# Kernel optimization log

Measured on AMD Instinct MI355X. Metric: run time of the kernel, lower is better.

Reference implementation:

```python
import jax, jax.numpy as jnp
import numpy as np

# Model dims (match init_kwargs cfg)
B, C_IN, L = 16, 3, 1024
D_MODEL, N_LAYERS = 256, 4
D_STATE, D_CONV, EXPAND = 16, 4, 2
D_INNER = EXPAND * D_MODEL            # 512
DT_RANK = (D_MODEL + 15) // 16        # 16 (mamba_ssm 'auto' rank)


def setup_inputs() -> dict:
    key = jax.random.key(0)
    ks = jax.random.split(key, 10)
    def rn(k, shape, scale):
        return jax.random.normal(k, shape, jnp.float32) * scale
    inp = {
        "x": jax.random.normal(ks[0], (B, C_IN, L), jnp.float32),
        # input stem: Conv1d(3 -> d_model, k=3, pad=1)
        "stem_w": rn(ks[1], (D_MODEL, C_IN, 3), 0.3),
        "stem_b": jnp.zeros((D_MODEL,), jnp.float32),
        # per-layer params, stacked on leading layer dim
        "norm_g": jnp.ones((N_LAYERS, D_MODEL), jnp.float32),
        "norm_b": jnp.zeros((N_LAYERS, D_MODEL), jnp.float32),
        "in_proj_w": rn(ks[2], (N_LAYERS, 2 * D_INNER, D_MODEL), 0.02),
        "conv_w": rn(ks[3], (N_LAYERS, D_INNER, D_CONV), 0.2),
        "conv_b": jnp.zeros((N_LAYERS, D_INNER), jnp.float32),
        "x_proj_w": rn(ks[4], (N_LAYERS, DT_RANK + 2 * D_STATE, D_INNER), 0.02),
        "dt_w": rn(ks[5], (N_LAYERS, D_INNER, DT_RANK), 0.05),
        "dt_b": jnp.full((N_LAYERS, D_INNER), -4.6, jnp.float32),  # softplus ~= 0.01
        "A_log": jnp.log(jnp.broadcast_to(
            jnp.arange(1, D_STATE + 1, dtype=jnp.float32), (N_LAYERS, D_INNER, D_STATE))),
        "Dp": jnp.ones((N_LAYERS, D_INNER), jnp.float32),
        "out_w": rn(ks[6], (N_LAYERS, D_MODEL, D_INNER), 0.02),
        # final norm + output head Conv1d(d_model -> 1, k=1)
        "fnorm_g": jnp.ones((D_MODEL,), jnp.float32),
        "fnorm_b": jnp.zeros((D_MODEL,), jnp.float32),
        "head_w": rn(ks[7], (1, D_MODEL), 0.05),
        "head_b": jnp.zeros((1,), jnp.float32),
    }
    return inp


def _layernorm(x, g, b, eps=1e-5):
    mu = jnp.mean(x, axis=-1, keepdims=True)
    var = jnp.mean((x - mu) ** 2, axis=-1, keepdims=True)
    return (x - mu) * jax.lax.rsqrt(var + eps) * g + b


def _silu(x):
    return x * jax.nn.sigmoid(x)


def _selective_scan(u, delta, A, Bm, Cm, D):
    # u, delta: [B, L, di]; Bm, Cm: [B, L, ds]; A: [di, ds]; D: [di]
    # h_t = exp(delta_t * A) * h_{t-1} + (delta_t * u_t) * B_t ; y_t = <C_t, h_t>
    def step(h, t):
        d_t, B_t, C_t, u_t = t  # [B,di], [B,ds], [B,ds], [B,di]
        h = h * jnp.exp(d_t[..., None] * A) + (d_t * u_t)[..., None] * B_t[:, None, :]
        return h, jnp.einsum('bds,bs->bd', h, C_t)
    h0 = jnp.zeros((u.shape[0], A.shape[0], A.shape[1]), u.dtype)
    xs = (jnp.moveaxis(delta, 1, 0), jnp.moveaxis(Bm, 1, 0),
          jnp.moveaxis(Cm, 1, 0), jnp.moveaxis(u, 1, 0))
    _, ys = jax.lax.scan(step, h0, xs)            # ys: [L, B, di]
    return jnp.moveaxis(ys, 0, 1) + u * D


def _mamba(x, in_w, cw, cb, xw, dtw, dtb, A_log, Dp, ow):
    # x: [B, L, d_model]
    xz = jnp.einsum('bld,ed->ble', x, in_w)       # [B, L, 2*di]
    xin, z = jnp.split(xz, 2, axis=-1)
    # causal depthwise conv over time
    xc = jnp.moveaxis(xin, 1, 2)                  # [B, di, L]
    xc = jax.lax.conv_general_dilated(
        xc, cw[:, None, :], (1,), [(D_CONV - 1, 0)],
        feature_group_count=D_INNER,
        dimension_numbers=('NCH', 'OIH', 'NCH')) + cb[None, :, None]
    xin = _silu(jnp.moveaxis(xc, 1, 2))           # [B, L, di]
    proj = jnp.einsum('bld,ed->ble', xin, xw)     # [B, L, dt_rank + 2*ds]
    dt = proj[..., :DT_RANK]
    Bm = proj[..., DT_RANK:DT_RANK + D_STATE]
    Cm = proj[..., DT_RANK + D_STATE:]
    delta = jax.nn.softplus(jnp.einsum('blr,dr->bld', dt, dtw) + dtb)
    A = -jnp.exp(A_log)
    y = _selective_scan(xin, delta, A, Bm, Cm, Dp)
    y = y * _silu(z)
    return jnp.einsum('bld,od->blo', y, ow)       # [B, L, d_model]


def reference(x, stem_w, stem_b, norm_g, norm_b, in_proj_w, conv_w, conv_b,
              x_proj_w, dt_w, dt_b, A_log, Dp, out_w, fnorm_g, fnorm_b,
              head_w, head_b):
    # stem: Conv1d(k=3, same padding) + ReLU
    h = jax.lax.conv_general_dilated(
        x, stem_w, (1,), [(1, 1)],
        dimension_numbers=('NCH', 'OIH', 'NCH')) + stem_b[None, :, None]
    h = jax.nn.relu(h)
    h = jnp.moveaxis(h, 1, 2)                     # [B, L, d_model]
    for i in range(N_LAYERS):
        h = h + _mamba(_layernorm(h, norm_g[i], norm_b[i]),
                       in_proj_w[i], conv_w[i], conv_b[i], x_proj_w[i],
                       dt_w[i], dt_b[i], A_log[i], Dp[i], out_w[i])
    h = _layernorm(h, fnorm_g, fnorm_b)
    out = jnp.einsum('bld,od->blo', h, head_w) + head_b
    return jax.nn.sigmoid(jnp.moveaxis(out, 1, 2))  # [B, 1, L]
```

## Files before the change

kernel.cpp:

```cpp
#include <hip/hip_runtime.h>
#include <math.h>

#define BSZ 16
#define LQ 1024
#define DM 256
#define DI 512
#define NT (BSZ*LQ)

typedef __attribute__((ext_vector_type(8))) short short8;
typedef __attribute__((ext_vector_type(4))) short short4v;
typedef __attribute__((ext_vector_type(4))) float f32x4;

#define AS1(p) (const __attribute__((address_space(1))) void*)(p)
#define AS3(p) (__attribute__((address_space(3))) void*)(p)
#define GLOAD16(g, l) __builtin_amdgcn_global_load_lds(AS1(g), AS3(l), 16, 0, 0)

__device__ __forceinline__ short f2bf(float f) {
  union { float f; unsigned u; } a; a.f = f;
  unsigned r = (a.u + 0x7FFF + ((a.u >> 16) & 1)) >> 16;
  return (short)r;
}
__device__ __forceinline__ float bf2f(short s) {
  union { unsigned u; float f; } a; a.u = ((unsigned)(unsigned short)s) << 16;
  return a.f;
}

__global__ void stem_kernel(const float* __restrict__ x, const float* __restrict__ w,
                            const float* __restrict__ bias, float* __restrict__ h) {
  int idx = blockIdx.x * 256 + threadIdx.x;
  int d = idx & 255;
  int l = (idx >> 8) & 1023;
  int b = idx >> 18;
  float acc = bias[d];
#pragma unroll
  for (int c = 0; c < 3; c++) {
    const float* xr = x + (size_t)(b * 3 + c) * LQ;
    const float* wr = w + (size_t)(d * 3 + c) * 3;
#pragma unroll
    for (int k = 0; k < 3; k++) {
      int t = l + k - 1;
      if (t >= 0 && t < LQ) acc += xr[t] * wr[k];
    }
  }
  h[idx] = fmaxf(acc, 0.f);
}

#define WB_IN 262144
#define WB_XP 65536
#define WB_OUT 131072
#define WB_L (WB_IN + WB_XP + WB_OUT)

__global__ void convert_w(const float* __restrict__ in_w, const float* __restrict__ xp_w,
                          const float* __restrict__ out_w, short* __restrict__ wb) {
  int layer = blockIdx.y;
  int idx = blockIdx.x * 256 + threadIdx.x;
  short* dst = wb + (size_t)layer * WB_L;
  float v;
  if (idx < WB_IN) {
    v = in_w[(size_t)layer * WB_IN + idx];
  } else if (idx < WB_IN + WB_XP) {
    int k = idx - WB_IN; int row = k >> 9, col = k & 511;
    v = (row < 48) ? xp_w[(size_t)layer * 48 * 512 + row * 512 + col] : 0.f;
  } else {
    int k = idx - WB_IN - WB_XP;
    v = out_w[(size_t)layer * WB_OUT + k];
  }
  dst[idx] = f2bf(v);
}

__global__ void ln_kernel(const float* __restrict__ x, const float* __restrict__ g,
                          const float* __restrict__ bv, short* __restrict__ o) {
  int token = blockIdx.x * 4 + (threadIdx.x >> 6);
  int lane = threadIdx.x & 63;
  f32x4 v = *(const f32x4*)(x + (size_t)token * DM + lane * 4);
  float s = v[0] + v[1] + v[2] + v[3];
  float q = v[0]*v[0] + v[1]*v[1] + v[2]*v[2] + v[3]*v[3];
#pragma unroll
  for (int off = 32; off > 0; off >>= 1) {
    s += __shfl_xor(s, off, 64);
    q += __shfl_xor(q, off, 64);
  }
  float mu = s * (1.f / DM);
  float var = q * (1.f / DM) - mu * mu;
  float rs = rsqrtf(var + 1e-5f);
  f32x4 gg = *(const f32x4*)(g + lane * 4);
  f32x4 bb = *(const f32x4*)(bv + lane * 4);
  short4v ov;
#pragma unroll
  for (int k = 0; k < 4; k++) ov[k] = f2bf((v[k] - mu) * rs * gg[k] + bb[k]);
  *(short4v*)(o + (size_t)token * DM + lane * 4) = ov;
}

__global__ __launch_bounds__(256) void gemm_mfma_s16(
    const short* __restrict__ A, int K,
    const short* __restrict__ W,
    short* __restrict__ C0, int ld0,
    short* __restrict__ C1, int ld1,
    int split, int N) {
  __shared__ short As[128 * 32];
  __shared__ short Bs[128 * 32];
  int tid = threadIdx.x;
  int wave = tid >> 6, lane = tid & 63;
  int bm = blockIdx.y * 128, bn = blockIdx.x * 128;
  int wm = (wave >> 1) * 64, wn = (wave & 1) * 64;

  f32x4 acc[4][4];
#pragma unroll
  for (int i = 0; i < 4; i++)
#pragma unroll
    for (int j = 0; j < 4; j++) { acc[i][j][0] = 0.f; acc[i][j][1] = 0.f; acc[i][j][2] = 0.f; acc[i][j][3] = 0.f; }

  int srow = lane >> 2;
  int scol = (lane & 3) * 8;
  const short* Ag = A + (size_t)(bm + wave * 32 + srow) * K + scol;
  const short* Wg = W + (size_t)(bn + wave * 32 + srow) * K + scol;
  short* AsW = As + wave * 32 * 32;
  short* BsW = Bs + wave * 32 * 32;

  int fr = lane & 15;
  int kg = (lane >> 4) * 8;

  for (int k0 = 0; k0 < K; k0 += 32) {
    GLOAD16(Ag + k0,                    AsW);
    GLOAD16(Ag + k0 + (size_t)16 * K,   AsW + 16 * 32);
    GLOAD16(Wg + k0,                    BsW);
    GLOAD16(Wg + k0 + (size_t)16 * K,   BsW + 16 * 32);
    __syncthreads();

    short8 af[4], bf[4];
#pragma unroll
    for (int i = 0; i < 4; i++) af[i] = *(const short8*)&As[(wm + i * 16 + fr) * 32 + kg];
#pragma unroll
    for (int j = 0; j < 4; j++) bf[j] = *(const short8*)&Bs[(wn + j * 16 + fr) * 32 + kg];
#pragma unroll
    for (int i = 0; i < 4; i++)
#pragma unroll
      for (int j = 0; j < 4; j++)
        acc[i][j] = __builtin_amdgcn_mfma_f32_16x16x32_bf16(af[i], bf[j], acc[i][j], 0, 0, 0);
    __syncthreads();
  }

  int cn = lane & 15, cr = (lane >> 4) * 4;
#pragma unroll
  for (int i = 0; i < 4; i++) {
    int row0 = bm + wm + i * 16 + cr;
#pragma unroll
    for (int j = 0; j < 4; j++) {
      int col = bn + wn + j * 16 + cn;
      if (col < N) {
#pragma unroll
        for (int r = 0; r < 4; r++) {
          short* p = (col < split) ? (C0 + (size_t)(row0 + r) * ld0 + col)
                                   : (C1 + (size_t)(row0 + r) * ld1 + (col - split));
          *p = f2bf(acc[i][j][r]);
        }
      }
    }
  }
}

__global__ __launch_bounds__(256) void gemm_mfma64(
    const short* __restrict__ A, int K,
    const short* __restrict__ W,
    float* __restrict__ C, int ldc, int N, int accum) {
  __shared__ short As[64 * 64];
  __shared__ short Bs[64 * 64];
  int tid = threadIdx.x;
  int wave = tid >> 6, lane = tid & 63;
  int bm = blockIdx.y * 64, bn = blockIdx.x * 64;
  int wm = (wave >> 1) * 32, wn = (wave & 1) * 32;

  f32x4 acc[2][2];
#pragma unroll
  for (int i = 0; i < 2; i++)
#pragma unroll
    for (int j = 0; j < 2; j++) { acc[i][j][0] = 0.f; acc[i][j][1] = 0.f; acc[i][j][2] = 0.f; acc[i][j][3] = 0.f; }

  const short* Ag = A + (size_t)bm * K;
  const short* Wg = W + (size_t)bn * K;
  int fr = lane & 15;
  int kg = (lane >> 4) * 8;

  for (int k0 = 0; k0 < K; k0 += 64) {
#pragma unroll
    for (int i = 0; i < 2; i++) {
      int c = tid + i * 256;
      int row = c >> 3, kk = (c & 7) * 8;
      GLOAD16(Ag + (size_t)row * K + k0 + kk, As + c * 8);
      GLOAD16(Wg + (size_t)row * K + k0 + kk, Bs + c * 8);
    }
    __syncthreads();

#pragma unroll
    for (int ks = 0; ks < 2; ks++) {
      short8 af[2], bf[2];
#pragma unroll
      for (int i = 0; i < 2; i++) af[i] = *(const short8*)&As[(wm + i * 16 + fr) * 64 + ks * 32 + kg];
#pragma unroll
      for (int j = 0; j < 2; j++) bf[j] = *(const short8*)&Bs[(wn + j * 16 + fr) * 64 + ks * 32 + kg];
#pragma unroll
      for (int i = 0; i < 2; i++)
#pragma unroll
        for (int j = 0; j < 2; j++)
          acc[i][j] = __builtin_amdgcn_mfma_f32_16x16x32_bf16(af[i], bf[j], acc[i][j], 0, 0, 0);
    }
    __syncthreads();
  }

  int cn = lane & 15, cr = (lane >> 4) * 4;
#pragma unroll
  for (int i = 0; i < 2; i++) {
    int row0 = bm + wm + i * 16 + cr;
#pragma unroll
    for (int j = 0; j < 2; j++) {
      int col = bn + wn + j * 16 + cn;
      if (col < N) {
#pragma unroll
        for (int r = 0; r < 4; r++) {
          float v = acc[i][j][r];
          float* p = C + (size_t)(row0 + r) * ldc + col;
          if (accum) v += *p;
          *p = v;
        }
      }
    }
  }
}

__global__ void conv_silu_kernel(const short* __restrict__ xcb, const float* __restrict__ cw,
                                 const float* __restrict__ cb, short* __restrict__ xinb) {
  int idx = blockIdx.x * 256 + threadIdx.x;
  int d = idx & 511;
  int l = (idx >> 9) & 1023;
  int b = idx >> 19;
  float acc = cb[d];
  const short* base = xcb + (size_t)b * LQ * 512 + d;
#pragma unroll
  for (int k = 0; k < 4; k++) {
    int t = l + k - 3;
    if (t >= 0) acc += bf2f(base[(size_t)t * 512]) * cw[d * 4 + k];
  }
  float s = acc / (1.f + __expf(-acc));
  xinb[idx] = f2bf(s);
}

template <int CTRL>
__device__ __forceinline__ float dpp_add(float x) {
  int yi = __builtin_amdgcn_update_dpp(0, __float_as_int(x), CTRL, 0xF, 0xF, true);
  return x + __int_as_float(yi);
}
__device__ __forceinline__ float sum16(float x) {
  x = dpp_add<0xB1>(x);
  x = dpp_add<0x4E>(x);
  x = dpp_add<0x124>(x);
  x = dpp_add<0x128>(x);
  return x;
}

#define TCH 32
__global__ __launch_bounds__(256) void scan_kernel(
    const short* __restrict__ xinb, const float* __restrict__ proj,
    const short* __restrict__ zc,
    const float* __restrict__ dt_w, const float* __restrict__ dt_b,
    const float* __restrict__ A_log, const float* __restrict__ Dp,
    short* __restrict__ ybf) {
  int b  = blockIdx.x >> 5;
  int d0 = (blockIdx.x & 31) << 4;
  int tid = threadIdx.x;
  int ci = tid >> 4;
  int s  = tid & 15;
  int d = d0 + ci;

  __shared__ float sDt[32 * 20];
  __shared__ float sBT[16 * 36];
  __shared__ float sCT[16 * 36];
  __shared__ float sUT[16 * 36];
  __shared__ float sDU[16 * 36];
  __shared__ float sDel[16 * 36];
  __shared__ float sY[32 * 17];

  float Av = -__expf(A_log[(size_t)d * 16 + s]);
  f32x4 wv4[4];
#pragma unroll
  for (int k = 0; k < 4; k++) wv4[k] = *(const f32x4*)&dt_w[(size_t)d * 16 + k * 4];
  float db = dt_b[d];
  float Ddj = Dp[d0 + s];
  float h = 0.f;

  const float* projb = proj + (size_t)b * LQ * 48;
  const short* xinbb = xinb + (size_t)b * LQ * 512 + d0;
  const short* zcb   = zc   + (size_t)b * LQ * 512 + d0;
  short* ybb         = ybf  + (size_t)b * LQ * 512 + d0;

  int tt = tid >> 4, j = tid & 15;

  int tr[6], rr[6];
#pragma unroll
  for (int k = 0; k < 6; k++) { int idx = tid + k * 256; tr[k] = idx / 48; rr[k] = idx - tr[k] * 48; }

  float uv0, uv1, zv0, zv1;
  {
    float pjv[6];
#pragma unroll
    for (int k = 0; k < 6; k++) pjv[k] = projb[tid + k * 256];
    uv0 = bf2f(xinbb[(size_t)tt * 512 + j]);
    uv1 = bf2f(xinbb[(size_t)(tt + 16) * 512 + j]);
    zv0 = bf2f(zcb[(size_t)tt * 512 + j]);
    zv1 = bf2f(zcb[(size_t)(tt + 16) * 512 + j]);
#pragma unroll
    for (int k = 0; k < 6; k++) {
      int r = rr[k], t = tr[k];
      if (r < 16)      sDt[t * 20 + r] = pjv[k];
      else if (r < 32) sBT[(r - 16) * 36 + t] = pjv[k];
      else             sCT[(r - 32) * 36 + t] = pjv[k];
    }
    sUT[j * 36 + tt] = uv0;
    sUT[j * 36 + tt + 16] = uv1;
  }
  __syncthreads();

  const int NCH = LQ / TCH;
  for (int c = 0; c < NCH; c++) {
    int t0 = c * TCH;

    float pjn[6], un0 = 0.f, un1 = 0.f, zn0 = 0.f, zn1 = 0.f;
    if (c + 1 < NCH) {
      const float* g = projb + (t0 + TCH) * 48;
#pragma unroll
      for (int k = 0; k < 6; k++) pjn[k] = g[tid + k * 256];
      un0 = bf2f(xinbb[(size_t)(t0 + TCH + tt) * 512 + j]);
      un1 = bf2f(xinbb[(size_t)(t0 + TCH + tt + 16) * 512 + j]);
      zn0 = bf2f(zcb[(size_t)(t0 + TCH + tt) * 512 + j]);
      zn1 = bf2f(zcb[(size_t)(t0 + TCH + tt + 16) * 512 + j]);
    }

    {
      f32x4 a0 = *(const f32x4*)&sDt[s * 20 + 0];
      f32x4 a1 = *(const f32x4*)&sDt[s * 20 + 4];
      f32x4 a2 = *(const f32x4*)&sDt[s * 20 + 8];
      f32x4 a3 = *(const f32x4*)&sDt[s * 20 + 12];
      f32x4 b0 = *(const f32x4*)&sDt[(s + 16) * 20 + 0];
      f32x4 b1 = *(const f32x4*)&sDt[(s + 16) * 20 + 4];
      f32x4 b2 = *(const f32x4*)&sDt[(s + 16) * 20 + 8];
      f32x4 b3 = *(const f32x4*)&sDt[(s + 16) * 20 + 12];
      float dt0 = db, dt1 = db;
#pragma unroll
      for (int q = 0; q < 4; q++) {
        dt0 += a0[q] * wv4[0][q] + a1[q] * wv4[1][q] + a2[q] * wv4[2][q] + a3[q] * wv4[3][q];
        dt1 += b0[q] * wv4[0][q] + b1[q] * wv4[1][q] + b2[q] * wv4[2][q] + b3[q] * wv4[3][q];
      }
      float de0 = (dt0 > 15.f) ? dt0 : __logf(1.f + __expf(dt0));
      float de1 = (dt1 > 15.f) ? dt1 : __logf(1.f + __expf(dt1));
      float u0 = sUT[ci * 36 + s];
      float u1 = sUT[ci * 36 + s + 16];
      sDel[ci * 36 + s]      = de0;
      sDel[ci * 36 + s + 16] = de1;
      sDU[ci * 36 + s]       = de0 * u0;
      sDU[ci * 36 + s + 16]  = de1 * u1;
    }
    __syncthreads();

    {
      float ee[TCH], cin[TCH];
      f32x4 ct[8];
      {
        f32x4 dl[8], du8[8], bt[8];
#pragma unroll
        for (int k = 0; k < 8; k++) {
          dl[k]  = *(const f32x4*)&sDel[ci * 36 + k * 4];
          du8[k] = *(const f32x4*)&sDU[ci * 36 + k * 4];
          bt[k]  = *(const f32x4*)&sBT[s * 36 + k * 4];
          ct[k]  = *(const f32x4*)&sCT[s * 36 + k * 4];
        }
#pragma unroll
        for (int t = 0; t < TCH; t++) {
          ee[t] = __expf(dl[t >> 2][t & 3] * Av);
          cin[t] = du8[t >> 2][t & 3] * bt[t >> 2][t & 3];
        }
      }
      float pv0 = 0.f, pv1 = 0.f;
#pragma unroll
      for (int t = 0; t < TCH; t++) {
        h = h * ee[t] + cin[t];
        float p = sum16(h * ct[t >> 2][t & 3]);
        if (t < 16) pv0 = (s == t) ? p : pv0;
        else        pv1 = (s == (t - 16)) ? p : pv1;
      }
      sY[s * 17 + ci] = pv0;
      sY[(s + 16) * 17 + ci] = pv1;
    }
    __syncthreads();

    {
      float p0 = sY[tt * 17 + j];
      float p1 = sY[(tt + 16) * 17 + j];
      float y0 = p0 + uv0 * Ddj;
      float y1 = p1 + uv1 * Ddj;
      float g0 = zv0 / (1.f + __expf(-zv0));
      float g1 = zv1 / (1.f + __expf(-zv1));
      ybb[(size_t)(t0 + tt) * 512 + j] = f2bf(y0 * g0);
      ybb[(size_t)(t0 + tt + 16) * 512 + j] = f2bf(y1 * g1);
    }
    if (c + 1 < NCH) {
#pragma unroll
      for (int k = 0; k < 6; k++) {
        int r = rr[k], t = tr[k];
        if (r < 16)      sDt[t * 20 + r] = pjn[k];
        else if (r < 32) sBT[(r - 16) * 36 + t] = pjn[k];
        else             sCT[(r - 32) * 36 + t] = pjn[k];
      }
      sUT[j * 36 + tt] = un0;
      sUT[j * 36 + tt + 16] = un1;
      uv0 = un0; uv1 = un1; zv0 = zn0; zv1 = zn1;
    }
    __syncthreads();
  }
}

__global__ void head_kernel(const float* __restrict__ h, const float* __restrict__ g,
                            const float* __restrict__ bv, const float* __restrict__ hw,
                            const float* __restrict__ hb, float* __restrict__ out) {
  int token = blockIdx.x;
  int d = threadIdx.x;
  float v = h[(size_t)token * DM + d];
  float s = v, q = v * v;
#pragma unroll
  for (int off = 32; off > 0; off >>= 1) {
    s += __shfl_down(s, off, 64);
    q += __shfl_down(q, off, 64);
  }
  __shared__ float ss[4], qq[4], cc[4];
  int lane = d & 63, wid = d >> 6;
  if (lane == 0) { ss[wid] = s; qq[wid] = q; }
  __syncthreads();
  s = ss[0] + ss[1] + ss[2] + ss[3];
  q = qq[0] + qq[1] + qq[2] + qq[3];
  float mu = s * (1.f / DM);
  float var = q * (1.f / DM) - mu * mu;
  float rs = rsqrtf(var + 1e-5f);
  float xn = (v - mu) * rs * g[d] + bv[d];
  float c = xn * hw[d];
#pragma unroll
  for (int off = 32; off > 0; off >>= 1) c += __shfl_down(c, off, 64);
  if (lane == 0) cc[wid] = c;
  __syncthreads();
  if (threadIdx.x == 0) {
    float t = cc[0] + cc[1] + cc[2] + cc[3] + hb[0];
    out[token] = 1.f / (1.f + __expf(-t));
  }
}

extern "C" void kernel_launch(void* const* d_in, const int* in_sizes, int n_in,
                              void* d_out, int out_size, void* d_ws, size_t ws_size,
                              hipStream_t stream) {
  const float* x        = (const float*)d_in[0];
  const float* stem_w   = (const float*)d_in[1];
  const float* stem_b   = (const float*)d_in[2];
  const float* norm_g   = (const float*)d_in[3];
  const float* norm_b   = (const float*)d_in[4];
  const float* in_proj_w= (const float*)d_in[5];
  const float* conv_w   = (const float*)d_in[6];
  const float* conv_b   = (const float*)d_in[7];
  const float* x_proj_w = (const float*)d_in[8];
  const float* dt_w     = (const float*)d_in[9];
  const float* dt_b     = (const float*)d_in[10];
  const float* A_log    = (const float*)d_in[11];
  const float* Dp       = (const float*)d_in[12];
  const float* out_w    = (const float*)d_in[13];
  const float* fnorm_g  = (const float*)d_in[14];
  const float* fnorm_b  = (const float*)d_in[15];
  const float* head_w   = (const float*)d_in[16];
  const float* head_b   = (const float*)d_in[17];

  char* base = (char*)d_ws;
  float* h    = (float*)(base);
  short* xcb  = (short*)(base + ((size_t)16 << 20));
  short* zcb  = (short*)(base + ((size_t)32 << 20));
  short* xnb  = (short*)(base + ((size_t)48 << 20));
  short* xinb = (short*)(base + ((size_t)56 << 20));
  short* ybf  = (short*)(base + ((size_t)72 << 20));
  float* proj = (float*)(base + ((size_t)88 << 20));
  short* wb   = (short*)(base + ((size_t)91 << 20));

  stem_kernel<<<NT, 256, 0, stream>>>(x, stem_w, stem_b, h);

  dim3 gcw(WB_L / 256, 4);
  convert_w<<<gcw, 256, 0, stream>>>(in_proj_w, x_proj_w, out_w, wb);

  for (int i = 0; i < 4; i++) {
    const short* wbl = wb + (size_t)i * WB_L;

    ln_kernel<<<NT / 4, 256, 0, stream>>>(h, norm_g + i * DM, norm_b + i * DM, xnb);

    dim3 g1(8, NT / 128);
    gemm_mfma_s16<<<g1, 256, 0, stream>>>(xnb, 256, wbl, xcb, 512, zcb, 512, 512, 1024);

    conv_silu_kernel<<<NT * DI / 256, 256, 0, stream>>>(xcb, conv_w + i * DI * 4,
                                                        conv_b + i * DI, xinb);

    dim3 g2(1, NT / 64);
    gemm_mfma64<<<g2, 256, 0, stream>>>(xinb, 512, wbl + WB_IN, proj, 48, 48, 0);

    scan_kernel<<<512, 256, 0, stream>>>(xinb, proj, zcb,
                                         dt_w + (size_t)i * DI * 16, dt_b + i * DI,
                                         A_log + (size_t)i * DI * 16, Dp + i * DI, ybf);

    dim3 g3(4, NT / 64);
    gemm_mfma64<<<g3, 256, 0, stream>>>(ybf, 512, wbl + WB_IN + WB_XP, h, 256, 256, 1);
  }

  head_kernel<<<NT, 256, 0, stream>>>(h, fnorm_g, fnorm_b, head_w, head_b, (float*)d_out);
}
```

Before: 875.3 us.

## Fuse LayerNorm into in_proj GEMM and causal conv+SiLU into x_proj GEMM

Drops the standalone LayerNorm and depthwise conv kernels. The in_proj GEMM now normalizes its 128-row tile of h straight into a full-K LDS buffer. The x_proj GEMM now computes the 4-tap causal conv plus SiLU per tile, feeding the MFMAs from LDS and also writing xinb for the scan. This removes the xnb round trip and the separate conv pass over xcb. The cost is that each of the 8 column blocks of GEMM1 recomputes LN and re-reads its rows of h, and the larger LDS footprint (about 75KB) may lower occupancy. The x_proj weight buffer is shrunk to 64 padded rows to match.

```diff
diff --git a/kernel.cpp b/kernel.cpp
--- a/kernel.cpp
+++ b/kernel.cpp
@@ -46,7 +46,7 @@
 }
 
 #define WB_IN 262144
-#define WB_XP 65536
+#define WB_XP 32768
 #define WB_OUT 131072
 #define WB_L (WB_IN + WB_XP + WB_OUT)
 
@@ -68,68 +68,73 @@
   dst[idx] = f2bf(v);
 }
 
-__global__ void ln_kernel(const float* __restrict__ x, const float* __restrict__ g,
-                          const float* __restrict__ bv, short* __restrict__ o) {
-  int token = blockIdx.x * 4 + (threadIdx.x >> 6);
-  int lane = threadIdx.x & 63;
-  f32x4 v = *(const f32x4*)(x + (size_t)token * DM + lane * 4);
-  float s = v[0] + v[1] + v[2] + v[3];
-  float q = v[0]*v[0] + v[1]*v[1] + v[2]*v[2] + v[3]*v[3];
-#pragma unroll
-  for (int off = 32; off > 0; off >>= 1) {
-    s += __shfl_xor(s, off, 64);
-    q += __shfl_xor(q, off, 64);
-  }
-  float mu = s * (1.f / DM);
-  float var = q * (1.f / DM) - mu * mu;
-  float rs = rsqrtf(var + 1e-5f);
-  f32x4 gg = *(const f32x4*)(g + lane * 4);
-  f32x4 bb = *(const f32x4*)(bv + lane * 4);
-  short4v ov;
-#pragma unroll
-  for (int k = 0; k < 4; k++) ov[k] = f2bf((v[k] - mu) * rs * gg[k] + bb[k]);
-  *(short4v*)(o + (size_t)token * DM + lane * 4) = ov;
-}
-
-__global__ __launch_bounds__(256) void gemm_mfma_s16(
-    const short* __restrict__ A, int K,
+__global__ __launch_bounds__(256) void gemm1_ln(
+    const float* __restrict__ hin, const float* __restrict__ g, const float* __restrict__ bv,
     const short* __restrict__ W,
-    short* __restrict__ C0, int ld0,
-    short* __restrict__ C1, int ld1,
-    int split, int N) {
-  __shared__ short As[128 * 32];
+    short* __restrict__ C0, short* __restrict__ C1) {
+  __shared__ short As[128 * 264];
   __shared__ short Bs[128 * 32];
   int tid = threadIdx.x;
   int wave = tid >> 6, lane = tid & 63;
   int bm = blockIdx.y * 128, bn = blockIdx.x * 128;
   int wm = (wave >> 1) * 64, wn = (wave & 1) * 64;
 
+  {
+    int r = tid >> 1, hf = tid & 1;
+    const float* hr = hin + (size_t)(bm + r) * DM + hf * 128;
+    float s = 0.f, q = 0.f;
+#pragma unroll
+    for (int c = 0; c < 32; c++) {
+      f32x4 v = *(const f32x4*)(hr + c * 4);
+      s += v[0] + v[1] + v[2] + v[3];
+      q += v[0]*v[0] + v[1]*v[1] + v[2]*v[2] + v[3]*v[3];
+    }
+    s += __shfl_xor(s, 1, 64);
+    q += __shfl_xor(q, 1, 64);
+    float mu = s * (1.f / DM);
+    float rs = rsqrtf(q * (1.f / DM) - mu * mu + 1e-5f);
+    const float* gp = g + hf * 128;
+    const float* bp = bv + hf * 128;
+    short* dst = &As[r * 264 + hf * 128];
+#pragma unroll
+    for (int c = 0; c < 16; c++) {
+      f32x4 v0 = *(const f32x4*)(hr + c * 8);
+      f32x4 v1 = *(const f32x4*)(hr + c * 8 + 4);
+      f32x4 g0 = *(const f32x4*)(gp + c * 8);
+      f32x4 g1 = *(const f32x4*)(gp + c * 8 + 4);
+      f32x4 b0 = *(const f32x4*)(bp + c * 8);
+      f32x4 b1 = *(const f32x4*)(bp + c * 8 + 4);
+      short8 o;
+#pragma unroll
+      for (int k = 0; k < 4; k++) {
+        o[k]     = f2bf((v0[k] - mu) * rs * g0[k] + b0[k]);
+        o[k + 4] = f2bf((v1[k] - mu) * rs * g1[k] + b1[k]);
+      }
+      *(short8*)(dst + c * 8) = o;
+    }
+  }
+
   f32x4 acc[4][4];
 #pragma unroll
   for (int i = 0; i < 4; i++)
 #pragma unroll
-    for (int j = 0; j < 4; j++) { acc[i][j][0] = 0.f; acc[i][j][1] = 0.f; acc[i][j][2] = 0.f; acc[i][j][3] = 0.f; }
+    for (int j = 0; j < 4; j++) { acc[i][j][0]=0.f; acc[i][j][1]=0.f; acc[i][j][2]=0.f; acc[i][j][3]=0.f; }
 
   int srow = lane >> 2;
   int scol = (lane & 3) * 8;
-  const short* Ag = A + (size_t)(bm + wave * 32 + srow) * K + scol;
-  const short* Wg = W + (size_t)(bn + wave * 32 + srow) * K + scol;
-  short* AsW = As + wave * 32 * 32;
+  const short* Wg = W + (size_t)(bn + wave * 32 + srow) * DM + scol;
   short* BsW = Bs + wave * 32 * 32;
-
   int fr = lane & 15;
   int kg = (lane >> 4) * 8;
 
-  for (int k0 = 0; k0 < K; k0 += 32) {
-    GLOAD16(Ag + k0,                    AsW);
-    GLOAD16(Ag + k0 + (size_t)16 * K,   AsW + 16 * 32);
-    GLOAD16(Wg + k0,                    BsW);
-    GLOAD16(Wg + k0 + (size_t)16 * K,   BsW + 16 * 32);
+  for (int k0 = 0; k0 < DM; k0 += 32) {
+    GLOAD16(Wg + k0,                     BsW);
+    GLOAD16(Wg + k0 + (size_t)16 * DM,   BsW + 16 * 32);
     __syncthreads();
 
     short8 af[4], bf[4];
 #pragma unroll
-    for (int i = 0; i < 4; i++) af[i] = *(const short8*)&As[(wm + i * 16 + fr) * 32 + kg];
+    for (int i = 0; i < 4; i++) af[i] = *(const short8*)&As[(wm + i * 16 + fr) * 264 + k0 + kg];
 #pragma unroll
     for (int j = 0; j < 4; j++) bf[j] = *(const short8*)&Bs[(wn + j * 16 + fr) * 32 + kg];
 #pragma unroll
@@ -147,13 +152,112 @@
 #pragma unroll
     for (int j = 0; j < 4; j++) {
       int col = bn + wn + j * 16 + cn;
-      if (col < N) {
-#pragma unroll
-        for (int r = 0; r < 4; r++) {
-          short* p = (col < split) ? (C0 + (size_t)(row0 + r) * ld0 + col)
-                                   : (C1 + (size_t)(row0 + r) * ld1 + (col - split));
-          *p = f2bf(acc[i][j][r]);
-        }
+#pragma unroll
+      for (int r = 0; r < 4; r++) {
+        short* p = (col < 512) ? (C0 + (size_t)(row0 + r) * 512 + col)
+                               : (C1 + (size_t)(row0 + r) * 512 + (col - 512));
+        *p = f2bf(acc[i][j][r]);
+      }
+    }
+  }
+}
+
+__global__ __launch_bounds__(256) void gemm2_conv(
+    const short* __restrict__ xcb, const float* __restrict__ cw, const float* __restrict__ cb,
+    const short* __restrict__ W, short* __restrict__ xinb, float* __restrict__ proj) {
+  __shared__ short As[64 * 72];
+  __shared__ short Bs[64 * 64];
+  __shared__ float sCW[512 * 4];
+  __shared__ float sCB[512];
+  int tid = threadIdx.x;
+  int wave = tid >> 6, lane = tid & 63;
+  int bm = blockIdx.y * 64;
+  int wm = (wave >> 1) * 32, wn = (wave & 1) * 32;
+
+  for (int i = tid; i < 2048; i += 256) sCW[i] = cw[i];
+  for (int i = tid; i < 512; i += 256) sCB[i] = cb[i];
+  __syncthreads();
+
+  f32x4 acc[2][2];
+#pragma unroll
+  for (int i = 0; i < 2; i++)
+#pragma unroll
+    for (int j = 0; j < 2; j++) { acc[i][j][0]=0.f; acc[i][j][1]=0.f; acc[i][j][2]=0.f; acc[i][j][3]=0.f; }
+
+  int fr = lane & 15, kg = (lane >> 4) * 8;
+  int r = tid >> 2;
+  int cg = (tid & 3) * 16;
+  int t = bm + r;
+  int l = t & 1023;
+
+  for (int k0 = 0; k0 < 512; k0 += 64) {
+#pragma unroll
+    for (int i = 0; i < 2; i++) {
+      int c = tid + i * 256;
+      int row = c >> 3, kk = (c & 7) * 8;
+      GLOAD16(W + (size_t)row * 512 + k0 + kk, Bs + c * 8);
+    }
+    int ch0 = k0 + cg;
+    short8 x0[4], x1[4];
+#pragma unroll
+    for (int k = 0; k < 4; k++) {
+      if (l + k - 3 >= 0) {
+        const short* p = xcb + (size_t)(t + k - 3) * 512 + ch0;
+        x0[k] = *(const short8*)p;
+        x1[k] = *(const short8*)(p + 8);
+      } else {
+        x0[k] = (short8)0; x1[k] = (short8)0;
+      }
+    }
+    short8 o0, o1;
+#pragma unroll
+    for (int e = 0; e < 8; e++) {
+      int ca = ch0 + e, cbn = ch0 + 8 + e;
+      f32x4 wa = *(const f32x4*)&sCW[ca * 4];
+      f32x4 wbv = *(const f32x4*)&sCW[cbn * 4];
+      float aa = sCB[ca], ab = sCB[cbn];
+#pragma unroll
+      for (int k = 0; k < 4; k++) {
+        aa += bf2f(x0[k][e]) * wa[k];
+        ab += bf2f(x1[k][e]) * wbv[k];
+      }
+      aa = aa / (1.f + __expf(-aa));
+      ab = ab / (1.f + __expf(-ab));
+      o0[e] = f2bf(aa); o1[e] = f2bf(ab);
+    }
+    *(short8*)&As[r * 72 + cg] = o0;
+    *(short8*)&As[r * 72 + cg + 8] = o1;
+    *(short8*)(xinb + (size_t)t * 512 + ch0) = o0;
+    *(short8*)(xinb + (size_t)t * 512 + ch0 + 8) = o1;
+    __syncthreads();
+
+#pragma unroll
+    for (int ks = 0; ks < 2; ks++) {
+      short8 af[2], bf[2];
+#pragma unroll
+      for (int i = 0; i < 2; i++) af[i] = *(const short8*)&As[(wm + i * 16 + fr) * 72 + ks * 32 + kg];
+#pragma unroll
+      for (int j = 0; j < 2; j++) bf[j] = *(const short8*)&Bs[(wn + j * 16 + fr) * 64 + ks * 32 + kg];
+#pragma unroll
+      for (int i = 0; i < 2; i++)
+#pragma unroll
+        for (int j = 0; j < 2; j++)
+          acc[i][j] = __builtin_amdgcn_mfma_f32_16x16x32_bf16(af[i], bf[j], acc[i][j], 0, 0, 0);
+    }
+    __syncthreads();
+  }
+
+  int cn = lane & 15, cr = (lane >> 4) * 4;
+#pragma unroll
+  for (int i = 0; i < 2; i++) {
+    int row0 = bm + wm + i * 16 + cr;
+#pragma unroll
+    for (int j = 0; j < 2; j++) {
+      int col = wn + j * 16 + cn;
+      if (col < 48) {
+#pragma unroll
+        for (int rr2 = 0; rr2 < 4; rr2++)
+          proj[(size_t)(row0 + rr2) * 48 + col] = acc[i][j][rr2];
       }
     }
   }
@@ -174,7 +278,7 @@
 #pragma unroll
   for (int i = 0; i < 2; i++)
 #pragma unroll
-    for (int j = 0; j < 2; j++) { acc[i][j][0] = 0.f; acc[i][j][1] = 0.f; acc[i][j][2] = 0.f; acc[i][j][3] = 0.f; }
+    for (int j = 0; j < 2; j++) { acc[i][j][0]=0.f; acc[i][j][1]=0.f; acc[i][j][2]=0.f; acc[i][j][3]=0.f; }
 
   const short* Ag = A + (size_t)bm * K;
   const short* Wg = W + (size_t)bn * K;
@@ -225,23 +329,6 @@
       }
     }
   }
-}
-
-__global__ void conv_silu_kernel(const short* __restrict__ xcb, const float* __restrict__ cw,
-                                 const float* __restrict__ cb, short* __restrict__ xinb) {
-  int idx = blockIdx.x * 256 + threadIdx.x;
-  int d = idx & 511;
-  int l = (idx >> 9) & 1023;
-  int b = idx >> 19;
-  float acc = cb[d];
-  const short* base = xcb + (size_t)b * LQ * 512 + d;
-#pragma unroll
-  for (int k = 0; k < 4; k++) {
-    int t = l + k - 3;
-    if (t >= 0) acc += bf2f(base[(size_t)t * 512]) * cw[d * 4 + k];
-  }
-  float s = acc / (1.f + __expf(-acc));
-  xinb[idx] = f2bf(s);
 }
 
 template <int CTRL>
@@ -476,11 +563,10 @@
   float* h    = (float*)(base);
   short* xcb  = (short*)(base + ((size_t)16 << 20));
   short* zcb  = (short*)(base + ((size_t)32 << 20));
-  short* xnb  = (short*)(base + ((size_t)48 << 20));
-  short* xinb = (short*)(base + ((size_t)56 << 20));
-  short* ybf  = (short*)(base + ((size_t)72 << 20));
-  float* proj = (float*)(base + ((size_t)88 << 20));
-  short* wb   = (short*)(base + ((size_t)91 << 20));
+  short* xinb = (short*)(base + ((size_t)48 << 20));
+  short* ybf  = (short*)(base + ((size_t)64 << 20));
+  float* proj = (float*)(base + ((size_t)80 << 20));
+  short* wb   = (short*)(base + ((size_t)83 << 20));
 
   stem_kernel<<<NT, 256, 0, stream>>>(x, stem_w, stem_b, h);
 
@@ -490,16 +576,13 @@
   for (int i = 0; i < 4; i++) {
     const short* wbl = wb + (size_t)i * WB_L;
 
-    ln_kernel<<<NT / 4, 256, 0, stream>>>(h, norm_g + i * DM, norm_b + i * DM, xnb);
-
     dim3 g1(8, NT / 128);
-    gemm_mfma_s16<<<g1, 256, 0, stream>>>(xnb, 256, wbl, xcb, 512, zcb, 512, 512, 1024);
-
-    conv_silu_kernel<<<NT * DI / 256, 256, 0, stream>>>(xcb, conv_w + i * DI * 4,
-                                                        conv_b + i * DI, xinb);
+    gemm1_ln<<<g1, 256, 0, stream>>>(h, norm_g + i * DM, norm_b + i * DM,
+                                     wbl, xcb, zcb);
 
     dim3 g2(1, NT / 64);
-    gemm_mfma64<<<g2, 256, 0, stream>>>(xinb, 512, wbl + WB_IN, proj, 48, 48, 0);
+    gemm2_conv<<<g2, 256, 0, stream>>>(xcb, conv_w + i * DI * 4, conv_b + i * DI,
+                                       wbl + WB_IN, xinb, proj);
 
     scan_kernel<<<512, 256, 0, stream>>>(xinb, proj, zcb,
                                          dt_w + (size_t)i * DI * 16, dt_b + i * DI,
```

Result: no change. 887.6 us (+1.4%).
